# Kernel optimization log

Measured on AMD Instinct MI355X. Metric: run time of the kernel, lower is better.

Reference implementation:

```python
import jax, jax.numpy as jnp
import numpy as np

NUM_USER = 200000
NUM_ITEM = 400000
D = 64
NNZ = 6000000
GCN_LAYER = 3


def setup_inputs() -> dict:
    key = jax.random.key(0)
    k1, k2, k3, k4 = jax.random.split(key, 4)
    n_nodes = NUM_USER + NUM_ITEM
    adj_indices = jax.random.randint(k1, (2, NNZ), 0, n_nodes, dtype=jnp.int32)
    # normalized adjacency values are positive; mimic D^-1/2 A D^-1/2 scale
    adj_values = jax.random.uniform(k2, (NNZ,), dtype=jnp.float32) * 0.1
    user_emb = jax.random.normal(k3, (NUM_USER, D), dtype=jnp.float32) * 0.01
    item_emb = jax.random.normal(k4, (NUM_ITEM, D), dtype=jnp.float32) * 0.01
    return {
        "adj_values": adj_values,
        "user_emb": user_emb,
        "item_emb": item_emb,
        "adj_indices": adj_indices,
        "gcn_layer": GCN_LAYER,
    }


def reference(adj_values, user_emb, item_emb, adj_indices, gcn_layer):
    """LightGCN propagation: gcn_layer hops of SpMM, stack, mean, split."""
    num_user = user_emb.shape[0]
    n_nodes = num_user + item_emb.shape[0]
    row, col = adj_indices[0], adj_indices[1]

    ego = jnp.concatenate([user_emb, item_emb], axis=0)  # [N, D]
    layers = [ego]
    cur = ego
    for _ in range(gcn_layer):  # small fixed layer loop
        # SpMM: out[row] += vals * cur[col]
        msg = adj_values[:, None] * cur[col]  # [nnz, D]
        cur = jax.ops.segment_sum(msg, row, num_segments=n_nodes)  # [N, D]
        layers.append(cur)
    mean_emb = jnp.mean(jnp.stack(layers, axis=1), axis=1)  # [N, D]
    return mean_emb[:num_user], mean_emb[num_user:]
```

## Files before the change

kernel.cpp:

```cpp
#include <hip/hip_runtime.h>
#include <stdint.h>

#define NUM_USER 200000
#define NUM_ITEM 400000
#define NNODES   (NUM_USER + NUM_ITEM)
#define D        64
#define NNZ      6000000
#define ND       ((size_t)NNODES * D)

#define RPB       512
#define NBUCK     ((NNODES + RPB - 1) / RPB)
#define CAP       8192
#define CHUNK     8192

typedef float    f4 __attribute__((ext_vector_type(4)));
typedef uint32_t u4 __attribute__((ext_vector_type(4)));

__device__ __forceinline__ uint32_t bfr(float f) {
    uint32_t u = __float_as_uint(f);
    return (u + 0x7FFFu + ((u >> 16) & 1u)) >> 16;
}
__device__ __forceinline__ uint32_t pack2(float lo, float hi) {
    return (bfr(hi) << 16) | bfr(lo);
}
__device__ __forceinline__ float bl(uint32_t u) { return __uint_as_float(u << 16); }
__device__ __forceinline__ float bh(uint32_t u) { return __uint_as_float(u & 0xFFFF0000u); }

__global__ void k_cvt(const float* __restrict__ uemb, const float* __restrict__ iemb,
                      u4* __restrict__ ego_bf) {
    long long tid = (long long)blockIdx.x * blockDim.x + threadIdx.x;
    if (tid >= (long long)(ND / 8)) return;
    int node = (int)(tid >> 3);
    int seg = (int)(tid & 7);
    const f4* src = (node < NUM_USER)
        ? (const f4*)uemb + ((size_t)node << 4) + seg * 2
        : (const f4*)iemb + ((size_t)(node - NUM_USER) << 4) + seg * 2;
    f4 a = src[0], b = src[1];
    u4 o;
    o.x = pack2(a.x, a.y); o.y = pack2(a.z, a.w);
    o.z = pack2(b.x, b.y); o.w = pack2(b.z, b.w);
    ego_bf[tid] = o;
}


__global__ void k_coarse_hist(const int* __restrict__ rows, int* __restrict__ bcnt) {
    __shared__ int h[NBUCK];
    for (int i = threadIdx.x; i < NBUCK; i += blockDim.x) h[i] = 0;
    __syncthreads();
    int stride = gridDim.x * blockDim.x;
    for (int e = blockIdx.x * blockDim.x + threadIdx.x; e < NNZ; e += stride)
        atomicAdd(&h[rows[e] >> 9], 1);
    __syncthreads();
    for (int i = threadIdx.x; i < NBUCK; i += blockDim.x)
        if (h[i]) atomicAdd(&bcnt[i], h[i]);
}

__global__ void k_bucket_scan(const int* __restrict__ bcnt, int* __restrict__ bbase,
                              int* __restrict__ bcur, int* __restrict__ row_ptr) {
    __shared__ int tsum[1024];
    int t = threadIdx.x;
    int i0 = 2 * t, i1 = 2 * t + 1;
    int c0 = (i0 < NBUCK) ? bcnt[i0] : 0;
    int c1 = (i1 < NBUCK) ? bcnt[i1] : 0;
    tsum[t] = c0 + c1;
    __syncthreads();
    for (int off = 1; off < 1024; off <<= 1) {
        int v = (t >= off) ? tsum[t - off] : 0;
        __syncthreads();
        tsum[t] += v;
        __syncthreads();
    }
    int excl = (t == 0) ? 0 : tsum[t - 1];
    if (i0 < NBUCK) { bbase[i0] = excl;      bcur[i0] = excl; }
    if (i1 < NBUCK) { bbase[i1] = excl + c0; bcur[i1] = excl + c0; }
    if (t == 0) { bbase[NBUCK] = NNZ; row_ptr[NNODES] = NNZ; }
}

__global__ void k_coarse_scatter(const int* __restrict__ rows, const int* __restrict__ cols,
                                 const float* __restrict__ vals, int* __restrict__ bcur,
                                 uint64_t* __restrict__ edges) {
    __shared__ int cnt[NBUCK];
    __shared__ int start[NBUCK];
    int t = threadIdx.x;
    long long base = (long long)blockIdx.x * CHUNK;
    for (int i = t; i < NBUCK; i += blockDim.x) cnt[i] = 0;
    __syncthreads();
    for (int i = t; i < CHUNK; i += blockDim.x) {
        long long e = base + i;
        if (e < NNZ) atomicAdd(&cnt[rows[e] >> 9], 1);
    }
    __syncthreads();
    for (int b = t; b < NBUCK; b += blockDim.x) {
        int c = cnt[b];
        start[b] = c ? atomicAdd(&bcur[b], c) : 0;
    }
    __syncthreads();
    for (int i = t; i < NBUCK; i += blockDim.x) cnt[i] = 0;
    __syncthreads();
    for (int i = t; i < CHUNK; i += blockDim.x) {
        long long e = base + i;
        if (e >= NNZ) continue;
        int r = rows[e];
        int b = r >> 9;
        int pos = start[b] + atomicAdd(&cnt[b], 1);
        uint64_t packed = ((uint64_t)(uint32_t)__float_as_int(vals[e]) << 32)
                        | ((uint64_t)(r & (RPB - 1)) << 20)
                        | (uint32_t)cols[e];
        edges[pos] = packed;
    }
}

__global__ void k_bucket_sort(const int* __restrict__ bbase, uint64_t* __restrict__ edges,
                              int* __restrict__ row_ptr) {
    __shared__ uint64_t stage[CAP];
    __shared__ int hist[RPB];
    __shared__ int cur[RPB];
    int b = blockIdx.x;
    int t = threadIdx.x;
    int bb = bbase[b];
    int cnt = bbase[b + 1] - bb;
    for (int i = t; i < cnt; i += blockDim.x) stage[i] = edges[bb + i];
    for (int i = t; i < RPB; i += blockDim.x) hist[i] = 0;
    __syncthreads();
    for (int i = t; i < cnt; i += blockDim.x)
        atomicAdd(&hist[(uint32_t)(stage[i] >> 20) & (RPB - 1)], 1);
    __syncthreads();
    for (int off = 1; off < RPB; off <<= 1) {
        int v = (t >= off) ? hist[t - off] : 0;
        __syncthreads();
        hist[t] += v;
        __syncthreads();
    }
    int excl = (t == 0) ? 0 : hist[t - 1];
    long long row = (long long)b * RPB + t;
    if (row < NNODES) row_ptr[row] = bb + excl;
    cur[t] = excl;
    __syncthreads();
    for (int i = t; i < cnt; i += blockDim.x) {
        uint64_t e = stage[i];
        int lr = (uint32_t)(e >> 20) & (RPB - 1);
        int pos = atomicAdd(&cur[lr], 1);
        edges[bb + pos] = (e & 0xFFFFFFFF00000000ull) | (e & 0xFFFFFull);
    }
}


template<int EPI, bool FINAL>
__global__ void k_hop(const int* __restrict__ row_ptr,
                      const uint64_t* __restrict__ edges,
                      const u4* __restrict__ src_bf,
                      const u4* __restrict__ epi_bf,
                      void* __restrict__ dst) {
    constexpr int U = 16;
    int wave = (blockIdx.x * blockDim.x + threadIdx.x) >> 6;
    int lane = threadIdx.x & 63;
    int g = lane >> 3;
    int l = lane & 7;
    int r = wave * 8 + g;
    bool rv = (r < NNODES);
    int beg = rv ? row_ptr[r] : 0;
    int end = rv ? row_ptr[r + 1] : 0;
    float acc0[8], acc1[8];
    #pragma unroll
    for (int k = 0; k < 8; ++k) { acc0[k] = 0.f; acc1[k] = 0.f; }
    for (int j = beg; j < end; j += U) {
        uint64_t cv[U];
        bool act[U];
        #pragma unroll
        for (int u = 0; u < U; ++u) {
            act[u] = (j + u < end);
            if (act[u]) cv[u] = edges[j + u];
        }
        u4 s[U];
        #pragma unroll
        for (int u = 0; u < U; ++u) {
            if (act[u]) s[u] = src_bf[((size_t)((uint32_t)cv[u] & 0xFFFFFu) << 3) + l];
        }
        #pragma unroll
        for (int u = 0; u < U; ++u) {
            if (act[u]) {
                float v = __int_as_float((int)(cv[u] >> 32));
                float* a = (u & 1) ? acc1 : acc0;
                a[0] += v * bl(s[u].x); a[1] += v * bh(s[u].x);
                a[2] += v * bl(s[u].y); a[3] += v * bh(s[u].y);
                a[4] += v * bl(s[u].z); a[5] += v * bh(s[u].z);
                a[6] += v * bl(s[u].w); a[7] += v * bh(s[u].w);
            }
        }
    }
    if (!rv) return;
    float res[8];
    #pragma unroll
    for (int k = 0; k < 8; ++k) res[k] = acc0[k] + acc1[k];
    if (EPI >= 1) {
        u4 eg;
        if (EPI == 2) eg = __builtin_nontemporal_load(epi_bf + ((size_t)r << 3) + l);
        else          eg = epi_bf[((size_t)r << 3) + l];
        res[0] += bl(eg.x); res[1] += bh(eg.x);
        res[2] += bl(eg.y); res[3] += bh(eg.y);
        res[4] += bl(eg.z); res[5] += bh(eg.z);
        res[6] += bl(eg.w); res[7] += bh(eg.w);
    }
    if (FINAL) {
        f4 o0 = {res[0] * 0.25f, res[1] * 0.25f, res[2] * 0.25f, res[3] * 0.25f};
        f4 o1 = {res[4] * 0.25f, res[5] * 0.25f, res[6] * 0.25f, res[7] * 0.25f};
        f4* dp = (f4*)dst + ((size_t)r << 4) + l * 2;
        __builtin_nontemporal_store(o0, dp);
        __builtin_nontemporal_store(o1, dp + 1);
    } else {
        u4 o;
        o.x = pack2(res[0], res[1]); o.y = pack2(res[2], res[3]);
        o.z = pack2(res[4], res[5]); o.w = pack2(res[6], res[7]);
        *((u4*)dst + ((size_t)r << 3) + l) = o;
    }
}

extern "C" void kernel_launch(void* const* d_in, const int* in_sizes, int n_in,
                              void* d_out, int out_size, void* d_ws, size_t ws_size,
                              hipStream_t stream) {
    const float* vals = (const float*)d_in[0];
    const float* uemb = (const float*)d_in[1];
    const float* iemb = (const float*)d_in[2];
    const int*   rows = (const int*)d_in[3];
    const int*   cols = rows + NNZ;

    float* out = (float*)d_out;

    size_t off = 0;
    char* ws = (char*)d_ws;
    auto take = [&](size_t bytes) { char* p = ws + off; off += (bytes + 255) & ~(size_t)255; return p; };
    u4*       P       = (u4*)take((ND / 8) * sizeof(u4));
    u4*       Q       = (u4*)take((ND / 8) * sizeof(u4));
    int*      row_ptr = (int*)take((NNODES + 1) * sizeof(int));
    int*      bcnt    = (int*)take(NBUCK * sizeof(int));
    int*      bbase   = (int*)take((NBUCK + 1) * sizeof(int));
    int*      bcur    = (int*)take(NBUCK * sizeof(int));
    uint64_t* edges   = (uint64_t*)take((size_t)NNZ * sizeof(uint64_t));
    (void)ws_size;

    const long long cvt_threads = ND / 8;
    k_cvt<<<(int)((cvt_threads + 255) / 256), 256, 0, stream>>>(uemb, iemb, P);

    hipMemsetAsync(bcnt, 0, NBUCK * sizeof(int), stream);
    k_coarse_hist<<<512, 512, 0, stream>>>(rows, bcnt);
    k_bucket_scan<<<1, 1024, 0, stream>>>(bcnt, bbase, bcur, row_ptr);
    k_coarse_scatter<<<(NNZ + CHUNK - 1) / CHUNK, 512, 0, stream>>>(rows, cols, vals, bcur, edges);
    k_bucket_sort<<<NBUCK, RPB, 0, stream>>>(bbase, edges, row_ptr);

    const int hop_blocks = (NNODES + 31) / 32;
    k_hop<1, false><<<hop_blocks, 256, 0, stream>>>(row_ptr, edges, P, P, Q);
    k_hop<0, false><<<hop_blocks, 256, 0, stream>>>(row_ptr, edges, Q, nullptr, P);
    k_hop<2, true ><<<hop_blocks, 256, 0, stream>>>(row_ptr, edges, P, Q, out);
}
```

Baseline: 674.2 us.

## Replace single-pass bucket scatter with two-level super-bucket then fine-bucket scatter

Replaces the global histogram plus scatter into 1172 buckets with a two-level radix partition. The first pass scatters edges into 74 super-buckets (8192 rows each) while also counting the fine buckets. The second pass redistributes each super-bucket into its 16 fine buckets, with writes that stay local. The goal is to make scattered global writes more coalesced and to fold the separate histogram pass into the first scatter. The cost is an extra intermediate round-trip of 12-byte records, staged in the Q buffer, and fixed per-super-bucket capacities (CAP_S) that only hold for roughly uniform row distributions.

```diff
diff --git a/kernel.cpp b/kernel.cpp
--- a/kernel.cpp
+++ b/kernel.cpp
@@ -11,7 +11,11 @@
 #define RPB       512
 #define NBUCK     ((NNODES + RPB - 1) / RPB)
 #define CAP       8192
-#define CHUNK     8192
+#define NSUP      74
+#define FPS       16
+#define CAP_S     86016
+#define CHUNK1    16384
+#define CHUNK2    14336
 
 typedef float    f4 __attribute__((ext_vector_type(4)));
 typedef uint32_t u4 __attribute__((ext_vector_type(4)));
@@ -43,16 +47,52 @@
 }
 
 
-__global__ void k_coarse_hist(const int* __restrict__ rows, int* __restrict__ bcnt) {
-    __shared__ int h[NBUCK];
-    for (int i = threadIdx.x; i < NBUCK; i += blockDim.x) h[i] = 0;
-    __syncthreads();
-    int stride = gridDim.x * blockDim.x;
-    for (int e = blockIdx.x * blockDim.x + threadIdx.x; e < NNZ; e += stride)
-        atomicAdd(&h[rows[e] >> 9], 1);
-    __syncthreads();
-    for (int i = threadIdx.x; i < NBUCK; i += blockDim.x)
-        if (h[i]) atomicAdd(&bcnt[i], h[i]);
+__global__ void k_init(int* __restrict__ scur) {
+    int t = threadIdx.x;
+    if (t < NSUP) scur[t] = t * CAP_S;
+}
+
+__global__ void k_super_scatter(const int* __restrict__ rows, const int* __restrict__ cols,
+                                const float* __restrict__ vals,
+                                int* __restrict__ scur, int* __restrict__ bcnt,
+                                uint32_t* __restrict__ sup) {
+    __shared__ int scnt_l[NSUP];
+    __shared__ int sstart[NSUP];
+    __shared__ int fcnt_l[NBUCK];
+    int t = threadIdx.x;
+    long long base = (long long)blockIdx.x * CHUNK1;
+    for (int i = t; i < NSUP; i += blockDim.x) scnt_l[i] = 0;
+    for (int i = t; i < NBUCK; i += blockDim.x) fcnt_l[i] = 0;
+    __syncthreads();
+    for (int i = t; i < CHUNK1; i += blockDim.x) {
+        long long e = base + i;
+        if (e < NNZ) {
+            int r = rows[e];
+            atomicAdd(&scnt_l[r >> 13], 1);
+            atomicAdd(&fcnt_l[r >> 9], 1);
+        }
+    }
+    __syncthreads();
+    for (int s = t; s < NSUP; s += blockDim.x) {
+        int c = scnt_l[s];
+        sstart[s] = c ? atomicAdd(&scur[s], c) : 0;
+    }
+    for (int f = t; f < NBUCK; f += blockDim.x)
+        if (fcnt_l[f]) atomicAdd(&bcnt[f], fcnt_l[f]);
+    __syncthreads();
+    for (int i = t; i < NSUP; i += blockDim.x) scnt_l[i] = 0;
+    __syncthreads();
+    for (int i = t; i < CHUNK1; i += blockDim.x) {
+        long long e = base + i;
+        if (e >= NNZ) continue;
+        int r = rows[e];
+        int s = r >> 13;
+        int pos = sstart[s] + atomicAdd(&scnt_l[s], 1);
+        uint32_t* p = sup + (size_t)pos * 3;
+        p[0] = (uint32_t)r;
+        p[1] = (uint32_t)cols[e];
+        p[2] = (uint32_t)__float_as_int(vals[e]);
+    }
 }
 
 __global__ void k_bucket_scan(const int* __restrict__ bcnt, int* __restrict__ bbase,
@@ -76,37 +116,36 @@
     if (t == 0) { bbase[NBUCK] = NNZ; row_ptr[NNODES] = NNZ; }
 }
 
-__global__ void k_coarse_scatter(const int* __restrict__ rows, const int* __restrict__ cols,
-                                 const float* __restrict__ vals, int* __restrict__ bcur,
-                                 uint64_t* __restrict__ edges) {
-    __shared__ int cnt[NBUCK];
-    __shared__ int start[NBUCK];
-    int t = threadIdx.x;
-    long long base = (long long)blockIdx.x * CHUNK;
-    for (int i = t; i < NBUCK; i += blockDim.x) cnt[i] = 0;
-    __syncthreads();
-    for (int i = t; i < CHUNK; i += blockDim.x) {
-        long long e = base + i;
-        if (e < NNZ) atomicAdd(&cnt[rows[e] >> 9], 1);
-    }
-    __syncthreads();
-    for (int b = t; b < NBUCK; b += blockDim.x) {
-        int c = cnt[b];
-        start[b] = c ? atomicAdd(&bcur[b], c) : 0;
-    }
-    __syncthreads();
-    for (int i = t; i < NBUCK; i += blockDim.x) cnt[i] = 0;
-    __syncthreads();
-    for (int i = t; i < CHUNK; i += blockDim.x) {
-        long long e = base + i;
-        if (e >= NNZ) continue;
-        int r = rows[e];
-        int b = r >> 9;
-        int pos = start[b] + atomicAdd(&cnt[b], 1);
-        uint64_t packed = ((uint64_t)(uint32_t)__float_as_int(vals[e]) << 32)
-                        | ((uint64_t)(r & (RPB - 1)) << 20)
-                        | (uint32_t)cols[e];
-        edges[pos] = packed;
+__global__ void k_fine_scatter(const int* __restrict__ scur, const uint32_t* __restrict__ sup,
+                               int* __restrict__ bcur, uint64_t* __restrict__ edges) {
+    __shared__ int fcnt_l[FPS];
+    __shared__ int fstart[FPS];
+    int t = threadIdx.x;
+    int s = blockIdx.x / 6;
+    int c = blockIdx.x % 6;
+    int scnt = scur[s] - s * CAP_S;
+    int j0 = c * CHUNK2;
+    if (j0 >= scnt) return;
+    int j1 = min(scnt, j0 + CHUNK2);
+    int fine_base = s * FPS;
+    const uint32_t* sb = sup + (size_t)s * CAP_S * 3;
+    if (t < FPS) fcnt_l[t] = 0;
+    __syncthreads();
+    for (int i = j0 + t; i < j1; i += blockDim.x)
+        atomicAdd(&fcnt_l[(int)(sb[(size_t)i * 3] >> 9) - fine_base], 1);
+    __syncthreads();
+    if (t < FPS) {
+        int cc = fcnt_l[t];
+        fstart[t] = cc ? atomicAdd(&bcur[fine_base + t], cc) : 0;
+        fcnt_l[t] = 0;
+    }
+    __syncthreads();
+    for (int i = j0 + t; i < j1; i += blockDim.x) {
+        const uint32_t* p = sb + (size_t)i * 3;
+        uint32_t r = p[0], col = p[1], vb = p[2];
+        int f = (int)(r >> 9) - fine_base;
+        int pos = fstart[f] + atomicAdd(&fcnt_l[f], 1);
+        edges[pos] = ((uint64_t)vb << 32) | ((uint64_t)(r & (RPB - 1)) << 20) | col;
     }
 }
 
@@ -143,7 +182,6 @@
         edges[bb + pos] = (e & 0xFFFFFFFF00000000ull) | (e & 0xFFFFFull);
     }
 }
-
 
 template<int EPI, bool FINAL>
 __global__ void k_hop(const int* __restrict__ row_ptr,
@@ -235,16 +273,19 @@
     int*      bcnt    = (int*)take(NBUCK * sizeof(int));
     int*      bbase   = (int*)take((NBUCK + 1) * sizeof(int));
     int*      bcur    = (int*)take(NBUCK * sizeof(int));
+    int*      scur    = (int*)take(NSUP * sizeof(int));
     uint64_t* edges   = (uint64_t*)take((size_t)NNZ * sizeof(uint64_t));
     (void)ws_size;
+    uint32_t* sup = (uint32_t*)Q;
 
     const long long cvt_threads = ND / 8;
     k_cvt<<<(int)((cvt_threads + 255) / 256), 256, 0, stream>>>(uemb, iemb, P);
 
     hipMemsetAsync(bcnt, 0, NBUCK * sizeof(int), stream);
-    k_coarse_hist<<<512, 512, 0, stream>>>(rows, bcnt);
+    k_init<<<1, 128, 0, stream>>>(scur);
+    k_super_scatter<<<(NNZ + CHUNK1 - 1) / CHUNK1, 512, 0, stream>>>(rows, cols, vals, scur, bcnt, sup);
     k_bucket_scan<<<1, 1024, 0, stream>>>(bcnt, bbase, bcur, row_ptr);
-    k_coarse_scatter<<<(NNZ + CHUNK - 1) / CHUNK, 512, 0, stream>>>(rows, cols, vals, bcur, edges);
+    k_fine_scatter<<<NSUP * 6, 512, 0, stream>>>(scur, sup, bcur, edges);
     k_bucket_sort<<<NBUCK, RPB, 0, stream>>>(bbase, edges, row_ptr);
 
     const int hop_blocks = (NNODES + 31) / 32;
```

After: 612.9 us. 1.1x faster.
